# Performance work log

Hardware: AMD Instinct MI355X
Metric: run time of the kernel (lower is better)

The kernel has to match this reference:

```python
import jax, jax.numpy as jnp
import numpy as np

N = 100000      # num nodes
E = 1600000     # num edges
DIN, H, DOUT = 64, 128, 64
EPS = 1e-5


def setup_inputs() -> dict:
    key = jax.random.key(0)
    ks = jax.random.split(key, 16)
    def w(k, shape):
        fan_in = shape[0]
        return jax.random.normal(k, shape, dtype=jnp.float32) / np.sqrt(fan_in)
    return {
        "x": jax.random.normal(ks[0], (N, DIN), dtype=jnp.float32),
        "edge_index": jax.random.randint(ks[1], (2, E), 0, N, dtype=jnp.int32),
        "W1": w(ks[2], (DIN, H)),  "b1": jnp.zeros((H,), jnp.float32),
        "W2": w(ks[3], (H, H)),    "b2": jnp.zeros((H,), jnp.float32),
        "W3": w(ks[4], (H, DOUT)), "b3": jnp.zeros((DOUT,), jnp.float32),
        "g1": jnp.ones((H,), jnp.float32),  "be1": jnp.zeros((H,), jnp.float32),
        "g2": jnp.ones((H,), jnp.float32),  "be2": jnp.zeros((H,), jnp.float32),
        "Ws1": w(ks[5], (DIN, H)),  "bs1": jnp.zeros((H,), jnp.float32),
        "Ws2": w(ks[6], (H, DOUT)), "bs2": jnp.zeros((DOUT,), jnp.float32),
    }


def _layer_norm(h, g, b):
    m = jnp.mean(h, axis=-1, keepdims=True)
    v = jnp.mean(jnp.square(h - m), axis=-1, keepdims=True)
    return (h - m) * jax.lax.rsqrt(v + EPS) * g + b


def reference(x, edge_index, W1, b1, W2, b2, W3, b3, g1, be1, g2, be2, Ws1, bs1, Ws2, bs2):
    n = x.shape[0]
    # GCNConv: add self-loops, symmetric deg^{-1/2} normalization (PyG default)
    loop = jnp.arange(n, dtype=edge_index.dtype)
    src = jnp.concatenate([edge_index[0], loop])  # [E+N]
    dst = jnp.concatenate([edge_index[1], loop])
    deg = jax.ops.segment_sum(jnp.ones_like(dst, dtype=x.dtype), dst, num_segments=n)
    dinv = jax.lax.rsqrt(deg)  # deg >= 1 thanks to self-loops
    norm = (dinv[src] * dinv[dst])[:, None]  # [E+N, 1]

    def conv(h, W, b):
        hw = h @ W                                   # [n, dout]
        msg = hw[src] * norm                         # gather + scale
        return jax.ops.segment_sum(msg, dst, num_segments=n) + b

    # layer 1: conv -> LN -> relu -> +skip1(x)   (dropout is eval-mode identity)
    x1 = jax.nn.relu(_layer_norm(conv(x, W1, b1), g1, be1)) + (x @ Ws1 + bs1)
    # layer 2: conv -> LN -> relu -> +x1
    x2 = jax.nn.relu(_layer_norm(conv(x1, W2, b2), g2, be2)) + x1
    # layer 3: conv + skip2(x1)
    x3 = conv(x2, W3, b3) + (x1 @ Ws2 + bs2)
    return x3
```

## Files before the change

kernel.cpp:

```cpp
#include <hip/hip_runtime.h>

#define LN_EPS 1e-5f

typedef unsigned short ushortT;

__device__ __forceinline__ float4 ld4(const float* p) { return *reinterpret_cast<const float4*>(p); }
__device__ __forceinline__ void st4(float* p, float4 v) { *reinterpret_cast<float4*>(p) = v; }
__device__ __forceinline__ float bf2f(unsigned u) { return __uint_as_float(u << 16); }
__device__ __forceinline__ unsigned short f2bf(float f) {
    unsigned u = __float_as_uint(f);
    u += 0x7fffu + ((u >> 16) & 1u);
    return (unsigned short)(u >> 16);
}
__device__ __forceinline__ unsigned pack2(float a, float b) {
    return (unsigned)f2bf(a) | ((unsigned)f2bf(b) << 16);
}


__global__ __launch_bounds__(256) void k_zero_i32(int* __restrict__ p, int n) {
    int i = blockIdx.x * 256 + threadIdx.x;
    if (i < n) p[i] = 0;
}

__global__ __launch_bounds__(256) void k_count(const int* __restrict__ dst, int* __restrict__ counts, int E) {
    int i = blockIdx.x * 256 + threadIdx.x;
    if (i < E) atomicAdd(&counts[dst[i]], 1);
}

__global__ __launch_bounds__(256) void k_dinv(const int* __restrict__ counts, float* __restrict__ dinv, int n) {
    int i = blockIdx.x * 256 + threadIdx.x;
    if (i < n) dinv[i] = rsqrtf((float)(counts[i] + 1));
}

__global__ __launch_bounds__(512) void k_scan1(const int* __restrict__ counts, int* __restrict__ bsum, int n) {
    __shared__ int s[512];
    int idx = blockIdx.x * 512 + threadIdx.x;
    s[threadIdx.x] = (idx < n) ? counts[idx] : 0;
    __syncthreads();
    for (int d = 256; d > 0; d >>= 1) {
        if (threadIdx.x < d) s[threadIdx.x] += s[threadIdx.x + d];
        __syncthreads();
    }
    if (threadIdx.x == 0) bsum[blockIdx.x] = s[0];
}

__global__ __launch_bounds__(512) void k_scan2(int* __restrict__ bsum, int nb) {
    __shared__ int s[512];
    int t = threadIdx.x;
    int v = (t < nb) ? bsum[t] : 0;
    s[t] = v;
    __syncthreads();
    for (int d = 1; d < 512; d <<= 1) {
        int tv = (t >= d) ? s[t - d] : 0;
        __syncthreads();
        s[t] += tv;
        __syncthreads();
    }
    if (t < nb) bsum[t] = s[t] - v;
}

__global__ __launch_bounds__(512) void k_scan3(const int* __restrict__ counts, const int* __restrict__ bsum,
                                               int* __restrict__ offsets, int* __restrict__ cursor, int n) {
    __shared__ int s[512];
    int tid = threadIdx.x;
    int idx = blockIdx.x * 512 + tid;
    int v = (idx < n) ? counts[idx] : 0;
    s[tid] = v;
    __syncthreads();
    for (int d = 1; d < 512; d <<= 1) {
        int t = (tid >= d) ? s[tid - d] : 0;
        __syncthreads();
        s[tid] += t;
        __syncthreads();
    }
    if (idx < n) {
        int ex = s[tid] - v + bsum[blockIdx.x];
        offsets[idx] = ex;
        cursor[idx] = ex;
    }
}

__global__ __launch_bounds__(256) void k_fill(const int* __restrict__ src, const int* __restrict__ dst,
                                              const float* __restrict__ dinv, int* __restrict__ cursor,
                                              int* __restrict__ csr_src, float* __restrict__ csr_w, int E) {
    int i = blockIdx.x * 256 + threadIdx.x;
    if (i < E) {
        int d = dst[i], s = src[i];
        int p = atomicAdd(&cursor[d], 1);
        csr_src[p] = s;
        csr_w[p] = dinv[s];
    }
}


__global__ __launch_bounds__(256) void k_cvt_bf16(const float* __restrict__ in, ushortT* __restrict__ o, int n4) {
    int i = blockIdx.x * 256 + threadIdx.x;
    if (i < n4) {
        float4 v = ld4(in + (size_t)i * 4);
        uint2 pk;
        pk.x = pack2(v.x, v.y);
        pk.y = pack2(v.z, v.w);
        *reinterpret_cast<uint2*>(o + (size_t)i * 4) = pk;
    }
}


template <int C>
__global__ __launch_bounds__(256) void k_agg(const ushortT* __restrict__ t16,
                                             const int* __restrict__ rs, const int* __restrict__ re,
                                             const int* __restrict__ csr_src, const float* __restrict__ csr_w,
                                             const float* __restrict__ dinv, float* __restrict__ agg, int n) {
    constexpr int G = C / 8;
    constexpr int NPB = 256 / G;
    const int grp = threadIdx.x / G;
    const int sub = threadIdx.x % G;
    const int node = blockIdx.x * NPB + grp;
    if (node >= n) return;
    const float di = dinv[node];
    float a[8];
#pragma unroll
    for (int i = 0; i < 8; ++i) a[i] = 0.f;
    const ushortT* base = t16 + sub * 8;
    const int p0 = rs[node], p1 = re[node];

    auto acc8 = [&](uint4 v, float w) {
        a[0] = fmaf(bf2f(v.x & 0xffffu), w, a[0]); a[1] = fmaf(bf2f(v.x >> 16), w, a[1]);
        a[2] = fmaf(bf2f(v.y & 0xffffu), w, a[2]); a[3] = fmaf(bf2f(v.y >> 16), w, a[3]);
        a[4] = fmaf(bf2f(v.z & 0xffffu), w, a[4]); a[5] = fmaf(bf2f(v.z >> 16), w, a[5]);
        a[6] = fmaf(bf2f(v.w & 0xffffu), w, a[6]); a[7] = fmaf(bf2f(v.w >> 16), w, a[7]);
    };

    int p = p0;
    for (; p + 2 <= p1; p += 2) {
        int s0 = csr_src[p], s1 = csr_src[p + 1];
        float w0 = csr_w[p] * di, w1 = csr_w[p + 1] * di;
        uint4 v0 = *reinterpret_cast<const uint4*>(base + (size_t)s0 * C);
        uint4 v1 = *reinterpret_cast<const uint4*>(base + (size_t)s1 * C);
        acc8(v0, w0);
        acc8(v1, w1);
    }
    if (p < p1) {
        int s0 = csr_src[p];
        float w0 = csr_w[p] * di;
        uint4 v0 = *reinterpret_cast<const uint4*>(base + (size_t)s0 * C);
        acc8(v0, w0);
    }
    {
        uint4 v = *reinterpret_cast<const uint4*>(base + (size_t)node * C);
        acc8(v, di * di);
    }
    float* o = agg + (size_t)node * C + sub * 8;
    st4(o, make_float4(a[0], a[1], a[2], a[3]));
    st4(o + 4, make_float4(a[4], a[5], a[6], a[7]));
}


__global__ __launch_bounds__(256) void k_final(const ushortT* __restrict__ t16,
                                               const int* __restrict__ rs, const int* __restrict__ re,
                                               const int* __restrict__ csr_src, const float* __restrict__ csr_w,
                                               const float* __restrict__ dinv, const float* __restrict__ bias,
                                               float* __restrict__ out, int n) {
    constexpr int C = 64, G = 8, NPB = 32;
    const int grp = threadIdx.x / G;
    const int sub = threadIdx.x % G;
    const int node = blockIdx.x * NPB + grp;
    if (node >= n) return;
    const float di = dinv[node];
    float a[8];
#pragma unroll
    for (int i = 0; i < 8; ++i) a[i] = 0.f;
    const ushortT* base = t16 + sub * 8;
    const int p0 = rs[node], p1 = re[node];

    auto acc8 = [&](uint4 v, float w) {
        a[0] = fmaf(bf2f(v.x & 0xffffu), w, a[0]); a[1] = fmaf(bf2f(v.x >> 16), w, a[1]);
        a[2] = fmaf(bf2f(v.y & 0xffffu), w, a[2]); a[3] = fmaf(bf2f(v.y >> 16), w, a[3]);
        a[4] = fmaf(bf2f(v.z & 0xffffu), w, a[4]); a[5] = fmaf(bf2f(v.z >> 16), w, a[5]);
        a[6] = fmaf(bf2f(v.w & 0xffffu), w, a[6]); a[7] = fmaf(bf2f(v.w >> 16), w, a[7]);
    };

    int p = p0;
    for (; p + 2 <= p1; p += 2) {
        int s0 = csr_src[p], s1 = csr_src[p + 1];
        float w0 = csr_w[p] * di, w1 = csr_w[p + 1] * di;
        uint4 v0 = *reinterpret_cast<const uint4*>(base + (size_t)s0 * C);
        uint4 v1 = *reinterpret_cast<const uint4*>(base + (size_t)s1 * C);
        acc8(v0, w0);
        acc8(v1, w1);
    }
    if (p < p1) {
        int s0 = csr_src[p];
        float w0 = csr_w[p] * di;
        uint4 v0 = *reinterpret_cast<const uint4*>(base + (size_t)s0 * C);
        acc8(v0, w0);
    }
    {
        uint4 v = *reinterpret_cast<const uint4*>(base + (size_t)node * C);
        acc8(v, di * di);
    }
    float* o = out + (size_t)node * 64 + sub * 8;
    const float* b = bias + sub * 8;
    float4 c0 = ld4(o), c1 = ld4(o + 4);
    float4 b0 = ld4(b), b1 = ld4(b + 4);
    st4(o, make_float4(c0.x + a[0] + b0.x, c0.y + a[1] + b0.y,
                       c0.z + a[2] + b0.z, c0.w + a[3] + b0.w));
    st4(o + 4, make_float4(c1.x + a[4] + b1.x, c1.y + a[5] + b1.y,
                           c1.z + a[6] + b1.z, c1.w + a[7] + b1.w));
}


template <int K, int M, bool BF16OUT>
__global__ __launch_bounds__(256) void gemm_small(const float* __restrict__ in, const float* __restrict__ W,
                                                  const float* __restrict__ bias, void* __restrict__ outp,
                                                  int nrows) {
    constexpr int CG = M / 4;
    constexpr int RG = 256 / CG;
    constexpr int RPT = 4;
    constexpr int ROWS = RG * RPT;
    constexpr int KH = 64;
    constexpr int KP = K + 4;

    __shared__ float Wl[KH][M];
    __shared__ float Xl[ROWS][KP];

    const int tid = threadIdx.x;
    const int cg = tid % CG;
    const int rg = tid / CG;

    float4 bias4 = make_float4(0.f, 0.f, 0.f, 0.f);
    if (bias) bias4 = ld4(bias + cg * 4);

    for (int base = blockIdx.x * ROWS; base < nrows; base += gridDim.x * ROWS) {
        __syncthreads();
        constexpr int NV = ROWS * K / 4;
        for (int i = tid; i < NV; i += 256) {
            int r = i / (K / 4), c = i % (K / 4);
            int gr = base + r;
            float4 v = make_float4(0.f, 0.f, 0.f, 0.f);
            if (gr < nrows) v = ld4(in + (size_t)gr * K + c * 4);
            st4(&Xl[r][c * 4], v);
        }

        float4 acc[RPT];
#pragma unroll
        for (int r = 0; r < RPT; ++r) acc[r] = bias4;

        for (int kh = 0; kh < K; kh += KH) {
            __syncthreads();
            constexpr int WV = KH * M / 4;
            for (int i = tid; i < WV; i += 256) {
                int kk = i / (M / 4), c = i % (M / 4);
                st4(&Wl[kk][c * 4], ld4(W + (size_t)(kh + kk) * M + c * 4));
            }
            __syncthreads();
#pragma unroll 4
            for (int kk = 0; kk < KH; ++kk) {
                float4 w4 = ld4(&Wl[kk][cg * 4]);
#pragma unroll
                for (int r = 0; r < RPT; ++r) {
                    float xv = Xl[rg * RPT + r][kh + kk];
                    acc[r].x = fmaf(xv, w4.x, acc[r].x);
                    acc[r].y = fmaf(xv, w4.y, acc[r].y);
                    acc[r].z = fmaf(xv, w4.z, acc[r].z);
                    acc[r].w = fmaf(xv, w4.w, acc[r].w);
                }
            }
        }
#pragma unroll
        for (int r = 0; r < RPT; ++r) {
            int gr = base + rg * RPT + r;
            if (gr < nrows) {
                if (BF16OUT) {
                    uint2 pk;
                    pk.x = pack2(acc[r].x, acc[r].y);
                    pk.y = pack2(acc[r].z, acc[r].w);
                    *reinterpret_cast<uint2*>((ushortT*)outp + (size_t)gr * M + cg * 4) = pk;
                } else {
                    st4((float*)outp + (size_t)gr * M + cg * 4, acc[r]);
                }
            }
        }
    }
}


template <int K>
__global__ __launch_bounds__(256) void gemm_ln(const float* __restrict__ in, const float* __restrict__ W,
                                               const float* __restrict__ bias, const float* __restrict__ g,
                                               const float* __restrict__ be, const float* __restrict__ skip,
                                               float* __restrict__ out32, ushortT* __restrict__ out16,
                                               int nrows) {
    constexpr int M = 128;
    constexpr int RPT = 4;
    constexpr int ROWS = 32;
    constexpr int KH = 64;
    constexpr int KP = K + 4;

    __shared__ float Wl[KH][M];
    __shared__ float Xl[ROWS][KP];

    const int tid = threadIdx.x;
    const int cg = tid & 31;
    const int rg = tid >> 5;

    const float4 bias4 = ld4(bias + cg * 4);
    const float4 g4 = ld4(g + cg * 4);
    const float4 be4 = ld4(be + cg * 4);

    for (int base = blockIdx.x * ROWS; base < nrows; base += gridDim.x * ROWS) {
        __syncthreads();
        constexpr int NV = ROWS * K / 4;
        for (int i = tid; i < NV; i += 256) {
            int r = i / (K / 4), c = i % (K / 4);
            int gr = base + r;
            float4 v = make_float4(0.f, 0.f, 0.f, 0.f);
            if (gr < nrows) v = ld4(in + (size_t)gr * K + c * 4);
            st4(&Xl[r][c * 4], v);
        }

        float4 acc[RPT];
#pragma unroll
        for (int r = 0; r < RPT; ++r) acc[r] = bias4;

        for (int kh = 0; kh < K; kh += KH) {
            __syncthreads();
            constexpr int WV = KH * M / 4;
            for (int i = tid; i < WV; i += 256) {
                int kk = i / (M / 4), c = i % (M / 4);
                st4(&Wl[kk][c * 4], ld4(W + (size_t)(kh + kk) * M + c * 4));
            }
            __syncthreads();
#pragma unroll 4
            for (int kk = 0; kk < KH; ++kk) {
                float4 w4 = ld4(&Wl[kk][cg * 4]);
#pragma unroll
                for (int r = 0; r < RPT; ++r) {
                    float xv = Xl[rg * RPT + r][kh + kk];
                    acc[r].x = fmaf(xv, w4.x, acc[r].x);
                    acc[r].y = fmaf(xv, w4.y, acc[r].y);
                    acc[r].z = fmaf(xv, w4.z, acc[r].z);
                    acc[r].w = fmaf(xv, w4.w, acc[r].w);
                }
            }
        }

#pragma unroll
        for (int r = 0; r < RPT; ++r) {
            int gr = base + rg * RPT + r;
            if (gr >= nrows) continue;
            float4 a = acc[r];
            float sum = a.x + a.y + a.z + a.w;
#pragma unroll
            for (int m = 16; m > 0; m >>= 1) sum += __shfl_xor(sum, m, 32);
            const float mean = sum * (1.f / 128.f);
            float dx = a.x - mean, dy = a.y - mean, dz = a.z - mean, dw = a.w - mean;
            float sq = dx * dx + dy * dy + dz * dz + dw * dw;
#pragma unroll
            for (int m = 16; m > 0; m >>= 1) sq += __shfl_xor(sq, m, 32);
            const float rstd = rsqrtf(sq * (1.f / 128.f) + LN_EPS);
            float4 s4 = ld4(skip + (size_t)gr * 128 + cg * 4);
            float4 y;
            y.x = fmaxf(fmaf(dx * rstd, g4.x, be4.x), 0.f) + s4.x;
            y.y = fmaxf(fmaf(dy * rstd, g4.y, be4.y), 0.f) + s4.y;
            y.z = fmaxf(fmaf(dz * rstd, g4.z, be4.z), 0.f) + s4.z;
            y.w = fmaxf(fmaf(dw * rstd, g4.w, be4.w), 0.f) + s4.w;
            st4(out32 + (size_t)gr * 128 + cg * 4, y);
            if (out16) {
                uint2 pk;
                pk.x = pack2(y.x, y.y);
                pk.y = pack2(y.z, y.w);
                *reinterpret_cast<uint2*>(out16 + (size_t)gr * 128 + cg * 4) = pk;
            }
        }
    }
}


extern "C" void kernel_launch(void* const* d_in, const int* in_sizes, int n_in,
                              void* d_out, int out_size, void* d_ws, size_t ws_size,
                              hipStream_t stream) {
    const float* x   = (const float*)d_in[0];
    const int* eidx  = (const int*)d_in[1];
    const float* W1  = (const float*)d_in[2];
    const float* b1  = (const float*)d_in[3];
    const float* W2  = (const float*)d_in[4];
    const float* b2  = (const float*)d_in[5];
    const float* W3  = (const float*)d_in[6];
    const float* b3  = (const float*)d_in[7];
    const float* g1  = (const float*)d_in[8];
    const float* be1 = (const float*)d_in[9];
    const float* g2  = (const float*)d_in[10];
    const float* be2 = (const float*)d_in[11];
    const float* Ws1 = (const float*)d_in[12];
    const float* bs1 = (const float*)d_in[13];
    const float* Ws2 = (const float*)d_in[14];
    const float* bs2 = (const float*)d_in[15];
    float* out = (float*)d_out;

    const int N = in_sizes[0] / 64;
    const int E = in_sizes[1] / 2;
    const int* esrc = eidx;
    const int* edst = eidx + E;

    char* p = (char*)d_ws;
    auto alloc = [&](size_t bytes) -> char* {
        char* q = p;
        p += (bytes + 255) & ~(size_t)255;
        return q;
    };
    float* S      = (float*)alloc((size_t)N * 128 * 4);
    float* X2     = S;
    float* X1     = (float*)alloc((size_t)N * 128 * 4);
    char* R3      = alloc((size_t)N * 128 * 4);
    ushortT* x16  = (ushortT*)R3;
    float* agg0   = (float*)(R3 + (((size_t)N * 64 * 2 + 255) & ~(size_t)255));
    float* agg1   = (float*)R3;
    ushortT* X1_16  = (ushortT*)alloc((size_t)N * 128 * 2);
    ushortT* HW3_16 = (ushortT*)alloc((size_t)N * 64 * 2);
    int* csr_src  = (int*)alloc((size_t)E * 4);
    float* csr_w  = (float*)alloc((size_t)E * 4);
    int* counts   = (int*)alloc((size_t)N * 4);
    int* offsets  = (int*)alloc((size_t)N * 4);
    int* cursor   = (int*)alloc((size_t)N * 4);
    float* dinv   = (float*)alloc((size_t)N * 4);
    const int NB = (N + 511) / 512;
    int* bsum     = (int*)alloc((size_t)NB * 4);

    const int gN256 = (N + 255) / 256;
    const int gE256 = (E + 255) / 256;

    k_zero_i32<<<gN256, 256, 0, stream>>>(counts, N);
    k_count<<<gE256, 256, 0, stream>>>(edst, counts, E);
    k_dinv<<<gN256, 256, 0, stream>>>(counts, dinv, N);
    k_scan1<<<NB, 512, 0, stream>>>(counts, bsum, N);
    k_scan2<<<1, 512, 0, stream>>>(bsum, NB);
    k_scan3<<<NB, 512, 0, stream>>>(counts, bsum, offsets, cursor, N);
    k_fill<<<gE256, 256, 0, stream>>>(esrc, edst, dinv, cursor, csr_src, csr_w, E);

    k_cvt_bf16<<<(N * 16 + 255) / 256, 256, 0, stream>>>(x, x16, N * 16);
    k_agg<64><<<(N + 31) / 32, 256, 0, stream>>>(x16, offsets, cursor, csr_src, csr_w,
                                                 dinv, agg0, N);
    gemm_small<64, 128, false><<<(N + 31) / 32, 256, 0, stream>>>(x, Ws1, bs1, S, N);
    gemm_ln<64><<<(N + 31) / 32, 256, 0, stream>>>(agg0, W1, b1, g1, be1, S,
                                                   X1, X1_16, N);

    k_agg<128><<<(N + 15) / 16, 256, 0, stream>>>(X1_16, offsets, cursor, csr_src, csr_w,
                                                  dinv, agg1, N);
    gemm_ln<128><<<(N + 31) / 32, 256, 0, stream>>>(agg1, W2, b2, g2, be2, X1,
                                                    X2, (ushortT*)nullptr, N);

    gemm_small<128, 64, false><<<(N + 63) / 64, 256, 0, stream>>>(X1, Ws2, bs2, out, N);
    gemm_small<128, 64, true><<<(N + 63) / 64, 256, 0, stream>>>(X2, W3, nullptr, HW3_16, N);
    k_final<<<(N + 31) / 32, 256, 0, stream>>>(HW3_16, offsets, cursor, csr_src, csr_w,
                                               dinv, b3, out, N);
}
```

Before: 623.6 us.

## Fuse neighbor aggregation into GEMM+LayerNorm kernels and interleave CSR src/weight

The separate aggregation kernels for layers 1 and 2 are merged into the following GEMM+LayerNorm kernel. Each block gathers its nodes' neighbor sums directly into shared memory and then runs the matmul, LayerNorm, ReLU and skip add, so the fp32 aggregate buffers are no longer written to and read back from global memory. The CSR source indices and edge weights are also packed into one uint2 array, so each edge needs one 8-byte load instead of two separate loads. In exchange, the layer-2 fused kernel processes only 16 nodes per block, so each block reloads the full weight matrix for fewer rows, and the larger shared-memory footprint may lower occupancy during the latency-bound gather phase.

Result: no change. 633.6 us (+1.6%).

```diff
diff --git a/kernel.cpp b/kernel.cpp
--- a/kernel.cpp
+++ b/kernel.cpp
@@ -82,13 +82,15 @@
 
 __global__ __launch_bounds__(256) void k_fill(const int* __restrict__ src, const int* __restrict__ dst,
                                               const float* __restrict__ dinv, int* __restrict__ cursor,
-                                              int* __restrict__ csr_src, float* __restrict__ csr_w, int E) {
+                                              uint2* __restrict__ csr, int E) {
     int i = blockIdx.x * 256 + threadIdx.x;
     if (i < E) {
         int d = dst[i], s = src[i];
         int p = atomicAdd(&cursor[d], 1);
-        csr_src[p] = s;
-        csr_w[p] = dinv[s];
+        uint2 v;
+        v.x = (unsigned)s;
+        v.y = __float_as_uint(dinv[s]);
+        csr[p] = v;
     }
 }
 
@@ -105,59 +107,136 @@
 }
 
 
-template <int C>
-__global__ __launch_bounds__(256) void k_agg(const ushortT* __restrict__ t16,
-                                             const int* __restrict__ rs, const int* __restrict__ re,
-                                             const int* __restrict__ csr_src, const float* __restrict__ csr_w,
-                                             const float* __restrict__ dinv, float* __restrict__ agg, int n) {
-    constexpr int G = C / 8;
-    constexpr int NPB = 256 / G;
-    const int grp = threadIdx.x / G;
-    const int sub = threadIdx.x % G;
-    const int node = blockIdx.x * NPB + grp;
-    if (node >= n) return;
-    const float di = dinv[node];
-    float a[8];
-#pragma unroll
-    for (int i = 0; i < 8; ++i) a[i] = 0.f;
-    const ushortT* base = t16 + sub * 8;
-    const int p0 = rs[node], p1 = re[node];
-
-    auto acc8 = [&](uint4 v, float w) {
-        a[0] = fmaf(bf2f(v.x & 0xffffu), w, a[0]); a[1] = fmaf(bf2f(v.x >> 16), w, a[1]);
-        a[2] = fmaf(bf2f(v.y & 0xffffu), w, a[2]); a[3] = fmaf(bf2f(v.y >> 16), w, a[3]);
-        a[4] = fmaf(bf2f(v.z & 0xffffu), w, a[4]); a[5] = fmaf(bf2f(v.z >> 16), w, a[5]);
-        a[6] = fmaf(bf2f(v.w & 0xffffu), w, a[6]); a[7] = fmaf(bf2f(v.w >> 16), w, a[7]);
-    };
-
-    int p = p0;
-    for (; p + 2 <= p1; p += 2) {
-        int s0 = csr_src[p], s1 = csr_src[p + 1];
-        float w0 = csr_w[p] * di, w1 = csr_w[p + 1] * di;
-        uint4 v0 = *reinterpret_cast<const uint4*>(base + (size_t)s0 * C);
-        uint4 v1 = *reinterpret_cast<const uint4*>(base + (size_t)s1 * C);
-        acc8(v0, w0);
-        acc8(v1, w1);
-    }
-    if (p < p1) {
-        int s0 = csr_src[p];
-        float w0 = csr_w[p] * di;
-        uint4 v0 = *reinterpret_cast<const uint4*>(base + (size_t)s0 * C);
-        acc8(v0, w0);
-    }
+template <int K>
+__global__ __launch_bounds__(256) void k_agg_gemm_ln(
+        const ushortT* __restrict__ t16, const uint2* __restrict__ csr,
+        const int* __restrict__ rs, const int* __restrict__ re,
+        const float* __restrict__ dinv,
+        const float* __restrict__ W, const float* __restrict__ bias,
+        const float* __restrict__ g, const float* __restrict__ be,
+        const float* __restrict__ skip,
+        float* __restrict__ out32, ushortT* __restrict__ out16, int n) {
+    constexpr int M = 128;
+    constexpr int G = K / 8;
+    constexpr int NODES = 256 / G;
+    constexpr int RPT = NODES / 8;
+    constexpr int KP = K + 8;
+
+    __shared__ float Wl[64][M];
+    __shared__ float Xl[NODES][KP];
+
+    const int tid = threadIdx.x;
+
     {
-        uint4 v = *reinterpret_cast<const uint4*>(base + (size_t)node * C);
-        acc8(v, di * di);
-    }
-    float* o = agg + (size_t)node * C + sub * 8;
-    st4(o, make_float4(a[0], a[1], a[2], a[3]));
-    st4(o + 4, make_float4(a[4], a[5], a[6], a[7]));
+        const int grp = tid / G;
+        const int sub = tid % G;
+        const int node = blockIdx.x * NODES + grp;
+        float a[8];
+#pragma unroll
+        for (int i = 0; i < 8; ++i) a[i] = 0.f;
+
+        if (node < n) {
+            const float di = dinv[node];
+            const ushortT* base = t16 + sub * 8;
+            const int p0 = rs[node], p1 = re[node];
+
+            auto acc8 = [&](uint4 v, float w) {
+                a[0] = fmaf(bf2f(v.x & 0xffffu), w, a[0]); a[1] = fmaf(bf2f(v.x >> 16), w, a[1]);
+                a[2] = fmaf(bf2f(v.y & 0xffffu), w, a[2]); a[3] = fmaf(bf2f(v.y >> 16), w, a[3]);
+                a[4] = fmaf(bf2f(v.z & 0xffffu), w, a[4]); a[5] = fmaf(bf2f(v.z >> 16), w, a[5]);
+                a[6] = fmaf(bf2f(v.w & 0xffffu), w, a[6]); a[7] = fmaf(bf2f(v.w >> 16), w, a[7]);
+            };
+
+            int p = p0;
+            for (; p + 2 <= p1; p += 2) {
+                uint2 e0 = csr[p], e1 = csr[p + 1];
+                float w0 = __uint_as_float(e0.y) * di;
+                float w1 = __uint_as_float(e1.y) * di;
+                uint4 v0 = *reinterpret_cast<const uint4*>(base + (size_t)e0.x * K);
+                uint4 v1 = *reinterpret_cast<const uint4*>(base + (size_t)e1.x * K);
+                acc8(v0, w0);
+                acc8(v1, w1);
+            }
+            if (p < p1) {
+                uint2 e0 = csr[p];
+                float w0 = __uint_as_float(e0.y) * di;
+                uint4 v0 = *reinterpret_cast<const uint4*>(base + (size_t)e0.x * K);
+                acc8(v0, w0);
+            }
+            {
+                uint4 v = *reinterpret_cast<const uint4*>(base + (size_t)node * K);
+                acc8(v, di * di);
+            }
+        }
+        st4(&Xl[grp][sub * 8], make_float4(a[0], a[1], a[2], a[3]));
+        st4(&Xl[grp][sub * 8 + 4], make_float4(a[4], a[5], a[6], a[7]));
+    }
+
+    const int cg = tid & 31;
+    const int rg = tid >> 5;
+    const float4 bias4 = ld4(bias + cg * 4);
+    const float4 g4 = ld4(g + cg * 4);
+    const float4 be4 = ld4(be + cg * 4);
+
+    float4 acc[RPT];
+#pragma unroll
+    for (int r = 0; r < RPT; ++r) acc[r] = bias4;
+
+    for (int kh = 0; kh < K; kh += 64) {
+        __syncthreads();
+        for (int i = tid; i < 64 * M / 4; i += 256) {
+            int kk = i / (M / 4), c = i % (M / 4);
+            st4(&Wl[kk][c * 4], ld4(W + (size_t)(kh + kk) * M + c * 4));
+        }
+        __syncthreads();
+#pragma unroll 4
+        for (int kk = 0; kk < 64; ++kk) {
+            float4 w4 = ld4(&Wl[kk][cg * 4]);
+#pragma unroll
+            for (int r = 0; r < RPT; ++r) {
+                float xv = Xl[rg * RPT + r][kh + kk];
+                acc[r].x = fmaf(xv, w4.x, acc[r].x);
+                acc[r].y = fmaf(xv, w4.y, acc[r].y);
+                acc[r].z = fmaf(xv, w4.z, acc[r].z);
+                acc[r].w = fmaf(xv, w4.w, acc[r].w);
+            }
+        }
+    }
+
+#pragma unroll
+    for (int r = 0; r < RPT; ++r) {
+        int gr = blockIdx.x * NODES + rg * RPT + r;
+        if (gr >= n) continue;
+        float4 a = acc[r];
+        float sum = a.x + a.y + a.z + a.w;
+#pragma unroll
+        for (int m = 16; m > 0; m >>= 1) sum += __shfl_xor(sum, m, 32);
+        const float mean = sum * (1.f / 128.f);
+        float dx = a.x - mean, dy = a.y - mean, dz = a.z - mean, dw = a.w - mean;
+        float sq = dx * dx + dy * dy + dz * dz + dw * dw;
+#pragma unroll
+        for (int m = 16; m > 0; m >>= 1) sq += __shfl_xor(sq, m, 32);
+        const float rstd = rsqrtf(sq * (1.f / 128.f) + LN_EPS);
+        float4 s4 = ld4(skip + (size_t)gr * 128 + cg * 4);
+        float4 y;
+        y.x = fmaxf(fmaf(dx * rstd, g4.x, be4.x), 0.f) + s4.x;
+        y.y = fmaxf(fmaf(dy * rstd, g4.y, be4.y), 0.f) + s4.y;
+        y.z = fmaxf(fmaf(dz * rstd, g4.z, be4.z), 0.f) + s4.z;
+        y.w = fmaxf(fmaf(dw * rstd, g4.w, be4.w), 0.f) + s4.w;
+        st4(out32 + (size_t)gr * 128 + cg * 4, y);
+        if (out16) {
+            uint2 pk;
+            pk.x = pack2(y.x, y.y);
+            pk.y = pack2(y.z, y.w);
+            *reinterpret_cast<uint2*>(out16 + (size_t)gr * 128 + cg * 4) = pk;
+        }
+    }
 }
 
 
 __global__ __launch_bounds__(256) void k_final(const ushortT* __restrict__ t16,
                                                const int* __restrict__ rs, const int* __restrict__ re,
-                                               const int* __restrict__ csr_src, const float* __restrict__ csr_w,
+                                               const uint2* __restrict__ csr,
                                                const float* __restrict__ dinv, const float* __restrict__ bias,
                                                float* __restrict__ out, int n) {
     constexpr int C = 64, G = 8, NPB = 32;
@@ -181,17 +260,18 @@
 
     int p = p0;
     for (; p + 2 <= p1; p += 2) {
-        int s0 = csr_src[p], s1 = csr_src[p + 1];
-        float w0 = csr_w[p] * di, w1 = csr_w[p + 1] * di;
-        uint4 v0 = *reinterpret_cast<const uint4*>(base + (size_t)s0 * C);
-        uint4 v1 = *reinterpret_cast<const uint4*>(base + (size_t)s1 * C);
+        uint2 e0 = csr[p], e1 = csr[p + 1];
+        float w0 = __uint_as_float(e0.y) * di;
+        float w1 = __uint_as_float(e1.y) * di;
+        uint4 v0 = *reinterpret_cast<const uint4*>(base + (size_t)e0.x * C);
+        uint4 v1 = *reinterpret_cast<const uint4*>(base + (size_t)e1.x * C);
         acc8(v0, w0);
         acc8(v1, w1);
     }
     if (p < p1) {
-        int s0 = csr_src[p];
-        float w0 = csr_w[p] * di;
-        uint4 v0 = *reinterpret_cast<const uint4*>(base + (size_t)s0 * C);
+        uint2 e0 = csr[p];
+        float w0 = __uint_as_float(e0.y) * di;
+        uint4 v0 = *reinterpret_cast<const uint4*>(base + (size_t)e0.x * C);
         acc8(v0, w0);
     }
     {
@@ -278,98 +358,6 @@
                 } else {
                     st4((float*)outp + (size_t)gr * M + cg * 4, acc[r]);
                 }
-            }
-        }
-    }
-}
-
-
-template <int K>
-__global__ __launch_bounds__(256) void gemm_ln(const float* __restrict__ in, const float* __restrict__ W,
-                                               const float* __restrict__ bias, const float* __restrict__ g,
-                                               const float* __restrict__ be, const float* __restrict__ skip,
-                                               float* __restrict__ out32, ushortT* __restrict__ out16,
-                                               int nrows) {
-    constexpr int M = 128;
-    constexpr int RPT = 4;
-    constexpr int ROWS = 32;
-    constexpr int KH = 64;
-    constexpr int KP = K + 4;
-
-    __shared__ float Wl[KH][M];
-    __shared__ float Xl[ROWS][KP];
-
-    const int tid = threadIdx.x;
-    const int cg = tid & 31;
-    const int rg = tid >> 5;
-
-    const float4 bias4 = ld4(bias + cg * 4);
-    const float4 g4 = ld4(g + cg * 4);
-    const float4 be4 = ld4(be + cg * 4);
-
-    for (int base = blockIdx.x * ROWS; base < nrows; base += gridDim.x * ROWS) {
-        __syncthreads();
-        constexpr int NV = ROWS * K / 4;
-        for (int i = tid; i < NV; i += 256) {
-            int r = i / (K / 4), c = i % (K / 4);
-            int gr = base + r;
-            float4 v = make_float4(0.f, 0.f, 0.f, 0.f);
-            if (gr < nrows) v = ld4(in + (size_t)gr * K + c * 4);
-            st4(&Xl[r][c * 4], v);
-        }
-
-        float4 acc[RPT];
-#pragma unroll
-        for (int r = 0; r < RPT; ++r) acc[r] = bias4;
-
-        for (int kh = 0; kh < K; kh += KH) {
-            __syncthreads();
-            constexpr int WV = KH * M / 4;
-            for (int i = tid; i < WV; i += 256) {
-                int kk = i / (M / 4), c = i % (M / 4);
-                st4(&Wl[kk][c * 4], ld4(W + (size_t)(kh + kk) * M + c * 4));
-            }
-            __syncthreads();
-#pragma unroll 4
-            for (int kk = 0; kk < KH; ++kk) {
-                float4 w4 = ld4(&Wl[kk][cg * 4]);
-#pragma unroll
-                for (int r = 0; r < RPT; ++r) {
-                    float xv = Xl[rg * RPT + r][kh + kk];
-                    acc[r].x = fmaf(xv, w4.x, acc[r].x);
-                    acc[r].y = fmaf(xv, w4.y, acc[r].y);
-                    acc[r].z = fmaf(xv, w4.z, acc[r].z);
-                    acc[r].w = fmaf(xv, w4.w, acc[r].w);
-                }
-            }
-        }
-
-#pragma unroll
-        for (int r = 0; r < RPT; ++r) {
-            int gr = base + rg * RPT + r;
-            if (gr >= nrows) continue;
-            float4 a = acc[r];
-            float sum = a.x + a.y + a.z + a.w;
-#pragma unroll
-            for (int m = 16; m > 0; m >>= 1) sum += __shfl_xor(sum, m, 32);
-            const float mean = sum * (1.f / 128.f);
-            float dx = a.x - mean, dy = a.y - mean, dz = a.z - mean, dw = a.w - mean;
-            float sq = dx * dx + dy * dy + dz * dz + dw * dw;
-#pragma unroll
-            for (int m = 16; m > 0; m >>= 1) sq += __shfl_xor(sq, m, 32);
-            const float rstd = rsqrtf(sq * (1.f / 128.f) + LN_EPS);
-            float4 s4 = ld4(skip + (size_t)gr * 128 + cg * 4);
-            float4 y;
-            y.x = fmaxf(fmaf(dx * rstd, g4.x, be4.x), 0.f) + s4.x;
-            y.y = fmaxf(fmaf(dy * rstd, g4.y, be4.y), 0.f) + s4.y;
-            y.z = fmaxf(fmaf(dz * rstd, g4.z, be4.z), 0.f) + s4.z;
-            y.w = fmaxf(fmaf(dw * rstd, g4.w, be4.w), 0.f) + s4.w;
-            st4(out32 + (size_t)gr * 128 + cg * 4, y);
-            if (out16) {
-                uint2 pk;
-                pk.x = pack2(y.x, y.y);
-                pk.y = pack2(y.z, y.w);
-                *reinterpret_cast<uint2*>(out16 + (size_t)gr * 128 + cg * 4) = pk;
             }
         }
     }
@@ -411,14 +399,10 @@
     float* S      = (float*)alloc((size_t)N * 128 * 4);
     float* X2     = S;
     float* X1     = (float*)alloc((size_t)N * 128 * 4);
-    char* R3      = alloc((size_t)N * 128 * 4);
-    ushortT* x16  = (ushortT*)R3;
-    float* agg0   = (float*)(R3 + (((size_t)N * 64 * 2 + 255) & ~(size_t)255));
-    float* agg1   = (float*)R3;
+    ushortT* x16  = (ushortT*)alloc((size_t)N * 64 * 2);
     ushortT* X1_16  = (ushortT*)alloc((size_t)N * 128 * 2);
     ushortT* HW3_16 = (ushortT*)alloc((size_t)N * 64 * 2);
-    int* csr_src  = (int*)alloc((size_t)E * 4);
-    float* csr_w  = (float*)alloc((size_t)E * 4);
+    uint2* csr    = (uint2*)alloc((size_t)E * 8);
     int* counts   = (int*)alloc((size_t)N * 4);
     int* offsets  = (int*)alloc((size_t)N * 4);
     int* cursor   = (int*)alloc((size_t)N * 4);
@@ -435,22 +419,20 @@
     k_scan1<<<NB, 512, 0, stream>>>(counts, bsum, N);
     k_scan2<<<1, 512, 0, stream>>>(bsum, NB);
     k_scan3<<<NB, 512, 0, stream>>>(counts, bsum, offsets, cursor, N);
-    k_fill<<<gE256, 256, 0, stream>>>(esrc, edst, dinv, cursor, csr_src, csr_w, E);
+    k_fill<<<gE256, 256, 0, stream>>>(esrc, edst, dinv, cursor, csr, E);
 
     k_cvt_bf16<<<(N * 16 + 255) / 256, 256, 0, stream>>>(x, x16, N * 16);
-    k_agg<64><<<(N + 31) / 32, 256, 0, stream>>>(x16, offsets, cursor, csr_src, csr_w,
-                                                 dinv, agg0, N);
     gemm_small<64, 128, false><<<(N + 31) / 32, 256, 0, stream>>>(x, Ws1, bs1, S, N);
-    gemm_ln<64><<<(N + 31) / 32, 256, 0, stream>>>(agg0, W1, b1, g1, be1, S,
-                                                   X1, X1_16, N);
-
-    k_agg<128><<<(N + 15) / 16, 256, 0, stream>>>(X1_16, offsets, cursor, csr_src, csr_w,
-                                                  dinv, agg1, N);
-    gemm_ln<128><<<(N + 31) / 32, 256, 0, stream>>>(agg1, W2, b2, g2, be2, X1,
-                                                    X2, (ushortT*)nullptr, N);
+    k_agg_gemm_ln<64><<<(N + 31) / 32, 256, 0, stream>>>(x16, csr, offsets, cursor, dinv,
+                                                         W1, b1, g1, be1, S,
+                                                         X1, X1_16, N);
+
+    k_agg_gemm_ln<128><<<(N + 15) / 16, 256, 0, stream>>>(X1_16, csr, offsets, cursor, dinv,
+                                                          W2, b2, g2, be2, X1,
+                                                          X2, (ushortT*)nullptr, N);
 
     gemm_small<128, 64, false><<<(N + 63) / 64, 256, 0, stream>>>(X1, Ws2, bs2, out, N);
     gemm_small<128, 64, true><<<(N + 63) / 64, 256, 0, stream>>>(X2, W3, nullptr, HW3_16, N);
-    k_final<<<(N + 31) / 32, 256, 0, stream>>>(HW3_16, offsets, cursor, csr_src, csr_w,
+    k_final<<<(N + 31) / 32, 256, 0, stream>>>(HW3_16, offsets, cursor, csr,
                                                dinv, b3, out, N);
 }
```
